# Optimization experiments

Measured on AMD Instinct MI355X. Metric: run time of the kernel, lower is better.

The kernel has to match this reference:

```python
import jax, jax.numpy as jnp
import numpy as np

NBINS = 64  # covers floor(|8*randn|) up to ~6 sigma


def setup_inputs() -> dict:
    key = jax.random.key(0)
    k1, k2 = jax.random.split(key)
    B, T = 64, 524288
    # scale so |y_true| spans many integer 'decade' bins (0..~45)
    y_true = jax.random.normal(k1, (B, T, 1), dtype=jnp.float32) * 8.0
    y_pred = y_true + jax.random.normal(k2, (B, T, 1), dtype=jnp.float32) * 0.5
    return {"y_pred": y_pred, "y_true": y_true}


def reference(y_pred, y_true):
    eps = jnp.finfo(y_true.dtype).eps
    abs_true = jnp.maximum(jnp.abs(y_true), eps)           # [B,T,1]
    loss_per_sample = jnp.square(y_pred - y_true)          # L2 base loss

    # per-sample decade index (non-differentiable integer path, as in torch)
    d = jnp.clip(jnp.floor(abs_true[..., 0]).astype(jnp.int32), 0, NBINS - 1)  # [B,T]
    B = d.shape[0]
    rows = jnp.arange(B)[:, None]                          # [B,1]

    # per-sample histogram via scatter-add (replaces torch.unique + searchsorted loop)
    counts = jnp.zeros((B, NBINS), jnp.float32).at[rows, d].add(1.0)  # [B,NBINS]
    weights = (1.0 / counts)[rows, d][..., None]           # [B,T,1]

    weighted_loss = jnp.sum(loss_per_sample * weights) / jnp.sum(weights)
    return jnp.sqrt(weighted_loss)  # L2 branch returns sqrt
```

## Files before the change

kernel.cpp:

```cpp
#include <hip/hip_runtime.h>
#include <math.h>

#define NBINS     64
#define HOT       32
#define TPB       256
#define NCOPY     128
#define CHUNK     8192
#define ITERS     (CHUNK / 4 / TPB)
#define CNT_SHIFT 25
#define SUM_MASK  ((1u << CNT_SHIFT) - 1u)
#define FP_SCALE  16384.0f
#define INV_FP    (1.0 / 16384.0)

__device__ __forceinline__ void glob_dadd(double* p, double v) {
    unsafeAtomicAdd(p, v);
}

__global__ __launch_bounds__(TPB, 8) void fused_kernel(
    const float* __restrict__ y_pred, const float* __restrict__ y_true,
    unsigned int* __restrict__ counts, double* __restrict__ gsum, int T)
{
    __shared__ unsigned int lh[HOT * NCOPY];
    __shared__ unsigned int pcnt[HOT][9];
    __shared__ unsigned int psum[HOT][9];

    const int tid = threadIdx.x;
    const int row = blockIdx.y;
    const int cp  = tid >> 1;

    uint4* lh4 = (uint4*)lh;
    for (int i = tid; i < (HOT * NCOPY) / 4; i += TPB)
        lh4[i] = make_uint4(0u, 0u, 0u, 0u);
    __syncthreads();

    const long long base = (long long)row * T + (long long)blockIdx.x * CHUNK;
    const float4* __restrict__ pp = (const float4*)(y_pred + base);
    const float4* __restrict__ pt = (const float4*)(y_true + base);

#pragma unroll
    for (int k = 0; k < ITERS; ++k) {
        float4 vp = pp[tid + k * TPB];
        float4 vt = pt[tid + k * TPB];

        float f0 = (vp.x - vt.x) * (vp.x - vt.x);
        float f1 = (vp.y - vt.y) * (vp.y - vt.y);
        float f2 = (vp.z - vt.z) * (vp.z - vt.z);
        float f3 = (vp.w - vt.w) * (vp.w - vt.w);

        int s0 = min((int)fabsf(vt.x), NBINS - 1);
        int s1 = min((int)fabsf(vt.y), NBINS - 1);
        int s2 = min((int)fabsf(vt.z), NBINS - 1);
        int s3 = min((int)fabsf(vt.w), NBINS - 1);

        unsigned int q0 = (1u << CNT_SHIFT) + (unsigned int)(fminf(f0, 15.99f) * FP_SCALE + 0.5f);
        unsigned int q1 = (1u << CNT_SHIFT) + (unsigned int)(fminf(f1, 15.99f) * FP_SCALE + 0.5f);
        unsigned int q2 = (1u << CNT_SHIFT) + (unsigned int)(fminf(f2, 15.99f) * FP_SCALE + 0.5f);
        unsigned int q3 = (1u << CNT_SHIFT) + (unsigned int)(fminf(f3, 15.99f) * FP_SCALE + 0.5f);

        if (s0 < HOT) atomicAdd(&lh[s0 * NCOPY + cp], q0);
        else { atomicAdd(&counts[row*NBINS+s0], 1u); glob_dadd(&gsum[row*NBINS+s0], (double)f0); }
        if (s1 < HOT) atomicAdd(&lh[s1 * NCOPY + cp], q1);
        else { atomicAdd(&counts[row*NBINS+s1], 1u); glob_dadd(&gsum[row*NBINS+s1], (double)f1); }
        if (s2 < HOT) atomicAdd(&lh[s2 * NCOPY + cp], q2);
        else { atomicAdd(&counts[row*NBINS+s2], 1u); glob_dadd(&gsum[row*NBINS+s2], (double)f2); }
        if (s3 < HOT) atomicAdd(&lh[s3 * NCOPY + cp], q3);
        else { atomicAdd(&counts[row*NBINS+s3], 1u); glob_dadd(&gsum[row*NBINS+s3], (double)f3); }
    }
    __syncthreads();

    {
        const int b = tid & (HOT - 1);
        const int c = tid >> 5;
        unsigned int cnt = 0, fs = 0;
        const unsigned int* lrow = &lh[b * NCOPY + c * 16];
        for (int j = 0; j < 16; ++j) {
            unsigned int p = lrow[(j + b) & 15];
            cnt += p >> CNT_SHIFT;
            fs  += p & SUM_MASK;
        }
        pcnt[b][c] = cnt;
        psum[b][c] = fs;
    }
    __syncthreads();

    if (tid < HOT) {
        unsigned int C = 0;
        double S = 0.0;
        for (int c = 0; c < 8; ++c) { C += pcnt[tid][c]; S += (double)psum[tid][c]; }
        if (C) {
            atomicAdd(&counts[row * NBINS + tid], C);
            glob_dadd(&gsum[row * NBINS + tid], S * INV_FP);
        }
    }
}

__global__ __launch_bounds__(256) void final_kernel(
    const unsigned int* __restrict__ counts, const double* __restrict__ gsum,
    int n_cells, float* __restrict__ out)
{
    const int tid = threadIdx.x;
    double num = 0.0, den = 0.0;
    for (int i = tid; i < n_cells; i += 256) {
        unsigned int c = counts[i];
        if (c) { num += gsum[i] / (double)c; den += 1.0; }
    }

    __shared__ double snum[256];
    __shared__ double sden[256];
    snum[tid] = num;
    sden[tid] = den;
    __syncthreads();
    for (int s = 128; s > 0; s >>= 1) {
        if (tid < s) { snum[tid] += snum[tid + s]; sden[tid] += sden[tid + s]; }
        __syncthreads();
    }
    if (tid == 0) out[0] = (float)sqrt(snum[0] / sden[0]);
}

extern "C" void kernel_launch(void* const* d_in, const int* in_sizes, int n_in,
                              void* d_out, int out_size, void* d_ws, size_t ws_size,
                              hipStream_t stream)
{
    const float* y_pred = (const float*)d_in[0];
    const float* y_true = (const float*)d_in[1];
    float* out = (float*)d_out;

    const int total = in_sizes[0];
    const int B = 64;
    const int T = total / B;

    unsigned int* counts = (unsigned int*)d_ws;
    double* gsum = (double*)((char*)d_ws + (size_t)B * NBINS * sizeof(unsigned int));

    const int bpr = T / CHUNK;
    dim3 grid(bpr, B);

    hipMemsetAsync(d_ws, 0,
                   (size_t)B * NBINS * (sizeof(unsigned int) + sizeof(double)),
                   stream);
    fused_kernel<<<grid, TPB, 0, stream>>>(y_pred, y_true, counts, gsum, T);
    final_kernel<<<1, 256, 0, stream>>>(counts, gsum, B * NBINS, out);
}
```

Measured before the change: 60.96 us.

## Stream inputs through LDS with double-buffered global_load_lds and shrink histogram copies

Replaces the direct unrolled float4 global loads with per-wave asynchronous global-to-LDS DMA into a two-stage ping-pong buffer, synchronized with explicit vmcnt waits. The aim is to overlap the next chunk's fetch with the current chunk's histogram atomics. It also halves the LDS histogram copies (NCOPY 64, four threads per slot) and repacks the count/sum fixed-point format with a coarser scale, which frees LDS but loses some sum precision. Keeping only one step in flight per thread may lower memory-level parallelism compared with the fully unrolled prefetching loop it replaces.

```diff
diff --git a/kernel.cpp b/kernel.cpp
--- a/kernel.cpp
+++ b/kernel.cpp
@@ -4,43 +4,65 @@
 #define NBINS     64
 #define HOT       32
 #define TPB       256
-#define NCOPY     128
+#define NCOPY     64
 #define CHUNK     8192
-#define ITERS     (CHUNK / 4 / TPB)
-#define CNT_SHIFT 25
+#define STEP      1024
+#define NSTEP     (CHUNK / STEP)
+#define CNT_SHIFT 24
 #define SUM_MASK  ((1u << CNT_SHIFT) - 1u)
-#define FP_SCALE  16384.0f
-#define INV_FP    (1.0 / 16384.0)
+#define FP_SCALE  4096.0f
+#define INV_FP    (1.0 / 4096.0)
 
 __device__ __forceinline__ void glob_dadd(double* p, double v) {
     unsafeAtomicAdd(p, v);
 }
 
-__global__ __launch_bounds__(TPB, 8) void fused_kernel(
+__device__ __forceinline__ void dma16(const float4* g, void* lds_base) {
+    __builtin_amdgcn_global_load_lds(
+        (const __attribute__((address_space(1))) void*)g,
+        (__attribute__((address_space(3))) void*)lds_base, 16, 0, 0);
+}
+
+__global__ __launch_bounds__(TPB) void fused_kernel(
     const float* __restrict__ y_pred, const float* __restrict__ y_true,
     unsigned int* __restrict__ counts, double* __restrict__ gsum, int T)
 {
+    __shared__ float4 bufP[2][TPB];
+    __shared__ float4 bufT[2][TPB];
     __shared__ unsigned int lh[HOT * NCOPY];
     __shared__ unsigned int pcnt[HOT][9];
     __shared__ unsigned int psum[HOT][9];
 
-    const int tid = threadIdx.x;
-    const int row = blockIdx.y;
-    const int cp  = tid >> 1;
+    const int tid  = threadIdx.x;
+    const int row  = blockIdx.y;
+    const int cp   = tid >> 2;
+    const int woff = (tid >> 6) * 64 * 16;
 
-    uint4* lh4 = (uint4*)lh;
-    for (int i = tid; i < (HOT * NCOPY) / 4; i += TPB)
-        lh4[i] = make_uint4(0u, 0u, 0u, 0u);
+    for (int i = tid; i < HOT * NCOPY; i += TPB) lh[i] = 0u;
     __syncthreads();
 
     const long long base = (long long)row * T + (long long)blockIdx.x * CHUNK;
-    const float4* __restrict__ pp = (const float4*)(y_pred + base);
-    const float4* __restrict__ pt = (const float4*)(y_true + base);
+    const float4* __restrict__ pp4 = (const float4*)(y_pred + base);
+    const float4* __restrict__ pt4 = (const float4*)(y_true + base);
+
+    dma16(pp4 + tid, (char*)&bufP[0][0] + woff);
+    dma16(pt4 + tid, (char*)&bufT[0][0] + woff);
 
 #pragma unroll
-    for (int k = 0; k < ITERS; ++k) {
-        float4 vp = pp[tid + k * TPB];
-        float4 vt = pt[tid + k * TPB];
+    for (int s = 0; s < NSTEP; ++s) {
+        const int q = s & 1;
+        if (s + 1 < NSTEP) {
+            const int qn = (s + 1) & 1;
+            dma16(pp4 + (s + 1) * TPB + tid, (char*)&bufP[qn][0] + woff);
+            dma16(pt4 + (s + 1) * TPB + tid, (char*)&bufT[qn][0] + woff);
+            asm volatile("s_waitcnt vmcnt(2)" ::: "memory");
+        } else {
+            asm volatile("s_waitcnt vmcnt(0)" ::: "memory");
+        }
+        __builtin_amdgcn_sched_barrier(0);
+
+        float4 vp = bufP[q][tid];
+        float4 vt = bufT[q][tid];
 
         float f0 = (vp.x - vt.x) * (vp.x - vt.x);
         float f1 = (vp.y - vt.y) * (vp.y - vt.y);
@@ -72,9 +94,9 @@
         const int b = tid & (HOT - 1);
         const int c = tid >> 5;
         unsigned int cnt = 0, fs = 0;
-        const unsigned int* lrow = &lh[b * NCOPY + c * 16];
-        for (int j = 0; j < 16; ++j) {
-            unsigned int p = lrow[(j + b) & 15];
+        const unsigned int* lrow = &lh[b * NCOPY + c * 8];
+        for (int j = 0; j < 8; ++j) {
+            unsigned int p = lrow[(j + b) & 7];
             cnt += p >> CNT_SHIFT;
             fs  += p & SUM_MASK;
         }
```

Result: faster. 59.62 us (-2.2%).
